# Kernel tuning notes

Measured on AMD Instinct MI355X. Metric: run time of the kernel, lower is better.

Reference implementation:

```python
import jax, jax.numpy as jnp
import numpy as np

B, P, N, H, TD, E = 4, 12, 4096, 64, 128, 65536
EPS = 1e-5


def _layer_norm2d(x, w, b):
    # LayerNorm over last two dims [N, H] with elementwise affine of shape [N, H]
    mu = jnp.mean(x, axis=(-2, -1), keepdims=True)
    var = jnp.var(x, axis=(-2, -1), keepdims=True)
    return (x - mu) * jax.lax.rsqrt(var + EPS) * w + b


def _projection(x, w1, b1, w2, b2):
    return jax.nn.relu(x @ w1.T + b1) @ w2.T + b2


def _lg_conv(x, edge_index):
    # PyG LGConv: symmetric gcn_norm without self loops, then scatter-add.
    row, col = edge_index[0], edge_index[1]
    deg = jax.ops.segment_sum(jnp.ones(E, x.dtype), col, num_segments=N)  # in-degree
    dis = jnp.where(deg > 0, jax.lax.rsqrt(jnp.maximum(deg, 1.0)), 0.0)   # deg^{-1/2}
    norm = dis[row] * dis[col]                                            # [E]
    xt = jnp.moveaxis(x, 2, 0)                                            # [N, B, P, H]
    msgs = xt[row] * norm[:, None, None, None]                            # [E, B, P, H]
    out = jax.ops.segment_sum(msgs, col, num_segments=N)                  # [N, B, P, H]
    return jnp.moveaxis(out, 0, 2)                                        # [B, P, N, H]


def setup_inputs() -> dict:
    key = jax.random.key(0)
    ks = jax.random.split(key, 16)
    s = 0.05
    return {
        "x": jax.random.normal(ks[0], (B, P, N, H), dtype=jnp.float32),
        "edge_index": jax.random.randint(ks[1], (2, E), 0, N),
        "time": jax.random.normal(ks[2], (B, TD), dtype=jnp.float32),
        "cond": jax.random.normal(ks[3], (B, P, N, H), dtype=jnp.float32),
        # time_projection: Linear(TD->H), Linear(H->H)
        "tp_w1": jax.random.normal(ks[4], (H, TD), dtype=jnp.float32) * s,
        "tp_b1": jnp.zeros((H,), jnp.float32),
        "tp_w2": jax.random.normal(ks[5], (H, H), dtype=jnp.float32) * s,
        "tp_b2": jnp.zeros((H,), jnp.float32),
        # cond_projection: Linear(H->H), Linear(H->H)
        "cp_w1": jax.random.normal(ks[6], (H, H), dtype=jnp.float32) * s,
        "cp_b1": jnp.zeros((H,), jnp.float32),
        "cp_w2": jax.random.normal(ks[7], (H, H), dtype=jnp.float32) * s,
        "cp_b2": jnp.zeros((H,), jnp.float32),
        # LayerNorm affine params [N, H]
        "gn_w": jnp.ones((N, H), jnp.float32),
        "gn_b": jnp.zeros((N, H), jnp.float32),
        "tn_w": jnp.ones((N, H), jnp.float32),
        "tn_b": jnp.zeros((N, H), jnp.float32),
        # Conv2d(P, P, 1x1)
        "conv_w": jax.random.normal(ks[8], (P, P), dtype=jnp.float32) * s,
        "conv_b": jnp.zeros((P,), jnp.float32),
    }


def reference(x, edge_index, time, cond, tp_w1, tp_b1, tp_w2, tp_b2,
              cp_w1, cp_b1, cp_w2, cp_b2, gn_w, gn_b, tn_w, tn_b,
              conv_w, conv_b):
    t = _projection(time, tp_w1, tp_b1, tp_w2, tp_b2)[:, None, None, :]  # [B,1,1,H]
    c = _projection(cond, cp_w1, cp_b1, cp_w2, cp_b2)                    # [B,P,N,H]
    h = x + c
    h = _layer_norm2d(h, gn_w, gn_b)
    h = _lg_conv(h, edge_index)
    h = h + t
    h = _layer_norm2d(h, tn_w, tn_b)
    # 1x1 Conv2d over the periods (channel) axis
    h = jnp.einsum('bpnh,qp->bqnh', h, conv_w) + conv_b[None, :, None, None]
    return h
```

## Files before the change

### kernel.cpp

```cpp
#include <hip/hip_runtime.h>
#include <hip/hip_bf16.h>

#define Bc   4
#define Pc   12
#define Nc   4096
#define Hc   64
#define TDc  128
#define Ec   65536
#define BPc  48
#define Gg   6
#define NHc  (Nc*Hc)
#define ROWS (BPc*Nc)
#define EPSc 1e-5f

typedef float    f32x4 __attribute__((ext_vector_type(4)));
typedef _Float16 f16x2 __attribute__((ext_vector_type(2)));
typedef _Float16 f16x4 __attribute__((ext_vector_type(4)));
typedef _Float16 f16x8 __attribute__((ext_vector_type(8)));

__global__ void k_tproj(const float* __restrict__ timev,
                        const float* __restrict__ w1, const float* __restrict__ b1,
                        const float* __restrict__ w2, const float* __restrict__ b2,
                        float* __restrict__ t_out) {
    __shared__ float s_time[Bc * TDc];
    __shared__ float s_hid[Bc * Hc];
    int t = threadIdx.x;
    for (int i = t; i < Bc * TDc; i += 256) s_time[i] = timev[i];
    __syncthreads();
    int b = t >> 6, j = t & 63;
    float acc = b1[j];
    for (int k = 0; k < TDc; ++k) acc = fmaf(s_time[b * TDc + k], w1[j * TDc + k], acc);
    s_hid[b * Hc + j] = fmaxf(acc, 0.f);
    __syncthreads();
    float acc2 = b2[j];
    for (int k = 0; k < Hc; ++k) acc2 = fmaf(s_hid[b * Hc + k], w2[j * Hc + k], acc2);
    t_out[b * Hc + j] = acc2;
}

__global__ void k_deg(const int* __restrict__ col, int* __restrict__ deg) {
    int e = blockIdx.x * 256 + threadIdx.x;
    atomicAdd(&deg[col[e]], 1);
}

__global__ __launch_bounds__(1024) void k_scan(const int* __restrict__ deg,
                                               int* __restrict__ offs,
                                               int* __restrict__ cursor,
                                               float* __restrict__ dis) {
    __shared__ int part[1024];
    int t = threadIdx.x;
    int d0 = deg[t * 4], d1 = deg[t * 4 + 1], d2 = deg[t * 4 + 2], d3 = deg[t * 4 + 3];
    part[t] = d0 + d1 + d2 + d3;
    __syncthreads();
    for (int off = 1; off < 1024; off <<= 1) {
        int v = (t >= off) ? part[t - off] : 0;
        __syncthreads();
        part[t] += v;
        __syncthreads();
    }
    int base = (t ? part[t - 1] : 0);
    offs[t * 4]     = base;
    offs[t * 4 + 1] = base + d0;
    offs[t * 4 + 2] = base + d0 + d1;
    offs[t * 4 + 3] = base + d0 + d1 + d2;
    if (t == 1023) offs[4096] = part[1023];
    cursor[t * 4]     = base;
    cursor[t * 4 + 1] = base + d0;
    cursor[t * 4 + 2] = base + d0 + d1;
    cursor[t * 4 + 3] = base + d0 + d1 + d2;
    dis[t * 4]     = d0 > 0 ? rsqrtf((float)d0) : 0.f;
    dis[t * 4 + 1] = d1 > 0 ? rsqrtf((float)d1) : 0.f;
    dis[t * 4 + 2] = d2 > 0 ? rsqrtf((float)d2) : 0.f;
    dis[t * 4 + 3] = d3 > 0 ? rsqrtf((float)d3) : 0.f;
}

__global__ void k_fill(const int* __restrict__ ei, int* __restrict__ cursor,
                       const float* __restrict__ dis,
                       int2* __restrict__ csr2) {
    int e = blockIdx.x * 256 + threadIdx.x;
    int r = ei[e], c = ei[Ec + e];
    int pos = atomicAdd(&cursor[c], 1);
    int2 v;
    v.x = r;
    v.y = __float_as_int(dis[r] * dis[c]);
    csr2[pos] = v;
}

__global__ __launch_bounds__(256) void k_pack(const float* __restrict__ gnw,
                                              const float* __restrict__ gnb,
                                              f16x2* __restrict__ gpack) {
    int i = blockIdx.x * 256 + threadIdx.x;
    f16x2 v;
    v.x = (_Float16)gnw[i];
    v.y = (_Float16)gnb[i];
    gpack[i] = v;
}

__global__ __launch_bounds__(256) void k_gw(const int* __restrict__ offs,
                                            const int2* __restrict__ csr2,
                                            const f16x2* __restrict__ gpack,
                                            float* __restrict__ g1, float* __restrict__ g2) {
    int wv = threadIdx.x >> 6, lane = threadIdx.x & 63;
    int n = __builtin_amdgcn_readfirstlane(blockIdx.x * 4 + wv);
    int s0 = __builtin_amdgcn_readfirstlane(offs[n]);
    int s1 = __builtin_amdgcn_readfirstlane(offs[n + 1]);
    float a0 = 0.f, a1 = 0.f, a2 = 0.f, a3 = 0.f;
    float b0 = 0.f, b1 = 0.f, b2 = 0.f, b3 = 0.f;
    int i = s0;
    for (; i + 4 <= s1; i += 4) {
        int2 e0 = csr2[i], e1 = csr2[i + 1], e2 = csr2[i + 2], e3 = csr2[i + 3];
        f16x2 v0 = gpack[e0.x * Hc + lane];
        f16x2 v1 = gpack[e1.x * Hc + lane];
        f16x2 v2 = gpack[e2.x * Hc + lane];
        f16x2 v3 = gpack[e3.x * Hc + lane];
        float w0 = __int_as_float(e0.y), w1 = __int_as_float(e1.y);
        float w2 = __int_as_float(e2.y), w3 = __int_as_float(e3.y);
        a0 = fmaf(w0, (float)v0.x, a0); b0 = fmaf(w0, (float)v0.y, b0);
        a1 = fmaf(w1, (float)v1.x, a1); b1 = fmaf(w1, (float)v1.y, b1);
        a2 = fmaf(w2, (float)v2.x, a2); b2 = fmaf(w2, (float)v2.y, b2);
        a3 = fmaf(w3, (float)v3.x, a3); b3 = fmaf(w3, (float)v3.y, b3);
    }
    for (; i < s1; ++i) {
        int2 e = csr2[i];
        f16x2 v = gpack[e.x * Hc + lane];
        float w = __int_as_float(e.y);
        a0 = fmaf(w, (float)v.x, a0); b0 = fmaf(w, (float)v.y, b0);
    }
    g1[n * Hc + lane] = (a0 + a1) + (a2 + a3);
    g2[n * Hc + lane] = (b0 + b1) + (b2 + b3);
}

__global__ __launch_bounds__(256) void k_mlp(const float* __restrict__ cond,
                                             const float* __restrict__ x,
                                             const float* __restrict__ w1, const float* __restrict__ b1,
                                             const float* __restrict__ w2, const float* __restrict__ b2,
                                             const float* __restrict__ gnw,
                                             _Float16* __restrict__ Af, float* __restrict__ part1) {
    __shared__ __align__(16) _Float16 wlds[8192];
    __shared__ float blds[128];
    __shared__ __align__(16) _Float16 s_h[4][16][72];

    int tid  = threadIdx.x;
    int lane = tid & 63;
    int wv   = tid >> 6;
    int r = lane & 15, g = lane >> 4;
    int bp = blockIdx.x >> 5;
    int g4 = bp & 7, j6 = bp >> 3;
    int nbase = (blockIdx.x & 31) * 128;

    #pragma unroll
    for (int layer = 0; layer < 2; ++layer) {
        const float* wsrc = layer ? w2 : w1;
        #pragma unroll
        for (int v4 = 0; v4 < 4; ++v4) {
            int i4 = tid + v4 * 256;
            int j  = i4 >> 4;
            int kq = (i4 & 15) * 4;
            f32x4 v = *(const f32x4*)(wsrc + j * Hc + kq);
            int t = j >> 4, rr = j & 15, kk = kq >> 4, gg = (kq >> 2) & 3;
            int ln = gg * 16 + rr;
            *(f16x4*)&wlds[(((layer * 4 + t) * 4 + kk) * 64 + ln) * 4] =
                __builtin_convertvector(v, f16x4);
        }
    }
    if (tid < 64) blds[tid] = b1[tid];
    else if (tid < 128) blds[tid] = b2[tid - 64];
    __syncthreads();

    float s = 0.f, ss = 0.f;
    int blockRow = blockIdx.x * 128;
    int nl = lane >> 3, hq = (lane & 7) * 8;
    for (int c = 0; c < 2; ++c) {
        __syncthreads();
        int row = blockRow + wv * 32 + c * 16 + r;
        int n   = row & (Nc - 1);
        f32x4 bcf[4], x4[4], gw4[4];
        #pragma unroll
        for (int kk = 0; kk < 4; ++kk)
            bcf[kk] = *(const f32x4*)(cond + (size_t)row * Hc + kk * 16 + 4 * g);
        #pragma unroll
        for (int t = 0; t < 4; ++t) {
            x4[t]  = *(const f32x4*)(x + (size_t)row * Hc + 16 * t + 4 * g);
            gw4[t] = *(const f32x4*)(gnw + n * Hc + 16 * t + 4 * g);
        }
        f16x4 bc[4];
        #pragma unroll
        for (int kk = 0; kk < 4; ++kk) bc[kk] = __builtin_convertvector(bcf[kk], f16x4);
        f16x4 hB[4];
        #pragma unroll
        for (int t = 0; t < 4; ++t) {
            f32x4 acc = {0.f, 0.f, 0.f, 0.f};
            #pragma unroll
            for (int kk = 0; kk < 4; ++kk) {
                f16x4 a = *(const f16x4*)&wlds[((t * 4 + kk) * 64 + lane) * 4];
                acc = __builtin_amdgcn_mfma_f32_16x16x16f16(a, bc[kk], acc, 0, 0, 0);
            }
            acc += *(const f32x4*)&blds[16 * t + 4 * g];
            f32x4 h;
            h.x = fmaxf(acc.x, 0.f); h.y = fmaxf(acc.y, 0.f);
            h.z = fmaxf(acc.z, 0.f); h.w = fmaxf(acc.w, 0.f);
            hB[t] = __builtin_convertvector(h, f16x4);
        }
        #pragma unroll
        for (int t = 0; t < 4; ++t) {
            f32x4 acc = {0.f, 0.f, 0.f, 0.f};
            #pragma unroll
            for (int kk = 0; kk < 4; ++kk) {
                f16x4 a = *(const f16x4*)&wlds[((16 + t * 4 + kk) * 64 + lane) * 4];
                acc = __builtin_amdgcn_mfma_f32_16x16x16f16(a, hB[kk], acc, 0, 0, 0);
            }
            f32x4 o = acc + *(const f32x4*)&blds[64 + 16 * t + 4 * g] + x4[t];
            s  += o.x + o.y + o.z + o.w;
            ss += o.x * o.x + o.y * o.y + o.z * o.z + o.w * o.w;
            f32x4 av = o * gw4[t];
            *(f16x4*)&s_h[wv][r][16 * t + 4 * g] = __builtin_convertvector(av, f16x4);
        }
        #pragma unroll
        for (int p = 0; p < 2; ++p) {
            f16x8 v = *(const f16x8*)&s_h[wv][p * 8 + nl][hq];
            int nn = nbase + wv * 32 + c * 16 + p * 8 + nl;
            *(f16x8*)(Af + (((size_t)g4 * Nc + nn) * Gg + j6) * Hc + hq) = v;
        }
    }
    for (int off = 32; off; off >>= 1) { s += __shfl_down(s, off); ss += __shfl_down(ss, off); }
    if (lane == 0) {
        int idx = (blockIdx.x & 31) * 4 + wv;
        part1[(bp * 128 + idx) * 2]     = s;
        part1[(bp * 128 + idx) * 2 + 1] = ss;
    }
}

__global__ __launch_bounds__(256) void k_finalize(const float* __restrict__ part, int cnt,
                                                  float* __restrict__ murs) {
    int bp = blockIdx.x;
    float s = 0.f, ss = 0.f;
    for (int i = threadIdx.x; i < cnt; i += 256) {
        s  += part[(bp * cnt + i) * 2];
        ss += part[(bp * cnt + i) * 2 + 1];
    }
    __shared__ float ls[4], lss[4];
    for (int off = 32; off; off >>= 1) { s += __shfl_down(s, off); ss += __shfl_down(ss, off); }
    int w = threadIdx.x >> 6, l = threadIdx.x & 63;
    if (l == 0) { ls[w] = s; lss[w] = ss; }
    __syncthreads();
    if (threadIdx.x == 0) {
        s  = ls[0] + ls[1] + ls[2] + ls[3];
        ss = lss[0] + lss[1] + lss[2] + lss[3];
        float mu = s / (float)NHc;
        float var = ss / (float)NHc - mu * mu;
        murs[bp * 2]     = mu;
        murs[bp * 2 + 1] = rsqrtf(var + EPSc);
    }
}

__global__ __launch_bounds__(256) void k_gather(const int* __restrict__ offs,
                                                const int2* __restrict__ csr2,
                                                const _Float16* __restrict__ Af,
                                                const float* __restrict__ g1,
                                                const float* __restrict__ g2,
                                                const float* __restrict__ murs,
                                                const float* __restrict__ t_in,
                                                _Float16* __restrict__ h2f,
                                                float* __restrict__ part2) {
    int bid = blockIdx.x;
    int g   = bid & 7;
    int seq = bid >> 3;
    int wv = threadIdx.x >> 6, lane = threadIdx.x & 63;
    int n  = __builtin_amdgcn_readfirstlane(seq * 4 + wv);
    int jj = lane >> 3;
    int jc = jj < Gg ? jj : 0;
    int h0 = (lane & 7) * 8;
    const _Float16* base = Af + (size_t)g * (Nc * Gg * Hc) + jc * Hc + h0;
    int s0 = __builtin_amdgcn_readfirstlane(offs[n]);
    int s1 = __builtin_amdgcn_readfirstlane(offs[n + 1]);

    float acc[8];
    #pragma unroll
    for (int i = 0; i < 8; ++i) acc[i] = 0.f;

    int idx = s0;
    for (; idx + 4 <= s1; idx += 4) {
        int2 e0 = csr2[idx],     e1 = csr2[idx + 1];
        int2 e2 = csr2[idx + 2], e3 = csr2[idx + 3];
        f16x8 v0 = *(const f16x8*)(base + (size_t)e0.x * (Gg * Hc));
        f16x8 v1 = *(const f16x8*)(base + (size_t)e1.x * (Gg * Hc));
        f16x8 v2 = *(const f16x8*)(base + (size_t)e2.x * (Gg * Hc));
        f16x8 v3 = *(const f16x8*)(base + (size_t)e3.x * (Gg * Hc));
        float w0 = __int_as_float(e0.y), w1 = __int_as_float(e1.y);
        float w2 = __int_as_float(e2.y), w3 = __int_as_float(e3.y);
        #pragma unroll
        for (int i = 0; i < 8; ++i) {
            acc[i] = fmaf(w0, (float)v0[i], acc[i]);
            acc[i] = fmaf(w1, (float)v1[i], acc[i]);
            acc[i] = fmaf(w2, (float)v2[i], acc[i]);
            acc[i] = fmaf(w3, (float)v3[i], acc[i]);
        }
    }
    for (; idx < s1; ++idx) {
        int2 e = csr2[idx];
        f16x8 v = *(const f16x8*)(base + (size_t)e.x * (Gg * Hc));
        float w = __int_as_float(e.y);
        #pragma unroll
        for (int i = 0; i < 8; ++i) acc[i] = fmaf(w, (float)v[i], acc[i]);
    }

    int bp = g + 8 * jc;
    int b  = bp / Pc;
    float mu = murs[bp * 2], rs = murs[bp * 2 + 1];
    f32x4 g1a = *(const f32x4*)(g1 + n * Hc + h0);
    f32x4 g1b = *(const f32x4*)(g1 + n * Hc + h0 + 4);
    f32x4 g2a = *(const f32x4*)(g2 + n * Hc + h0);
    f32x4 g2b = *(const f32x4*)(g2 + n * Hc + h0 + 4);
    f32x4 tta = *(const f32x4*)(t_in + b * Hc + h0);
    f32x4 ttb = *(const f32x4*)(t_in + b * Hc + h0 + 4);
    f32x4 va, vb;
    va.x = rs * (acc[0] - mu * g1a.x) + g2a.x + tta.x;
    va.y = rs * (acc[1] - mu * g1a.y) + g2a.y + tta.y;
    va.z = rs * (acc[2] - mu * g1a.z) + g2a.z + tta.z;
    va.w = rs * (acc[3] - mu * g1a.w) + g2a.w + tta.w;
    vb.x = rs * (acc[4] - mu * g1b.x) + g2b.x + ttb.x;
    vb.y = rs * (acc[5] - mu * g1b.y) + g2b.y + ttb.y;
    vb.z = rs * (acc[6] - mu * g1b.z) + g2b.z + ttb.z;
    vb.w = rs * (acc[7] - mu * g1b.w) + g2b.w + ttb.w;

    float s  = (va.x + va.y) + (va.z + va.w) + (vb.x + vb.y) + (vb.z + vb.w);
    float ss = va.x * va.x + va.y * va.y + va.z * va.z + va.w * va.w
             + vb.x * vb.x + vb.y * vb.y + vb.z * vb.z + vb.w * vb.w;
    #pragma unroll
    for (int m = 4; m; m >>= 1) { s += __shfl_xor(s, m); ss += __shfl_xor(ss, m); }

    if (jj < Gg) {
        f16x8 hv;
        hv[0] = (_Float16)va.x; hv[1] = (_Float16)va.y;
        hv[2] = (_Float16)va.z; hv[3] = (_Float16)va.w;
        hv[4] = (_Float16)vb.x; hv[5] = (_Float16)vb.y;
        hv[6] = (_Float16)vb.z; hv[7] = (_Float16)vb.w;
        *(f16x8*)(h2f + (size_t)bp * NHc + n * Hc + h0) = hv;
        if ((lane & 7) == 0) {
            part2[((size_t)bp * Nc + n) * 2]     = s;
            part2[((size_t)bp * Nc + n) * 2 + 1] = ss;
        }
    }
}

__global__ __launch_bounds__(256) void k_conv(const _Float16* __restrict__ h2f,
                                              const float* __restrict__ murs,
                                              const float* __restrict__ tnw, const float* __restrict__ tnb,
                                              const float* __restrict__ cw, const float* __restrict__ cb,
                                              float* __restrict__ out) {
    int tid = blockIdx.x * 256 + threadIdx.x;
    int b  = tid >> 16;
    int i4 = tid & 65535;
    size_t e0 = (size_t)i4 * 4;
    float4 w4 = *(const float4*)(tnw + e0);
    float4 b4 = *(const float4*)(tnb + e0);
    float v[Pc][4];
    #pragma unroll
    for (int p = 0; p < Pc; ++p) {
        int bp = b * Pc + p;
        float mu = murs[bp * 2], rs = murs[bp * 2 + 1];
        f16x4 h = *(const f16x4*)(h2f + (size_t)bp * NHc + e0);
        v[p][0] = ((float)h.x - mu) * rs * w4.x + b4.x;
        v[p][1] = ((float)h.y - mu) * rs * w4.y + b4.y;
        v[p][2] = ((float)h.z - mu) * rs * w4.z + b4.z;
        v[p][3] = ((float)h.w - mu) * rs * w4.w + b4.w;
    }
    #pragma unroll
    for (int q = 0; q < Pc; ++q) {
        float cbq = cb[q];
        float o0 = cbq, o1 = cbq, o2 = cbq, o3 = cbq;
        #pragma unroll
        for (int p = 0; p < Pc; ++p) {
            float wqp = cw[q * Pc + p];
            o0 = fmaf(v[p][0], wqp, o0);
            o1 = fmaf(v[p][1], wqp, o1);
            o2 = fmaf(v[p][2], wqp, o2);
            o3 = fmaf(v[p][3], wqp, o3);
        }
        float4 o = {o0, o1, o2, o3};
        *(float4*)(out + (size_t)(b * Pc + q) * NHc + e0) = o;
    }
}

extern "C" void kernel_launch(void* const* d_in, const int* in_sizes, int n_in,
                              void* d_out, int out_size, void* d_ws, size_t ws_size,
                              hipStream_t stream) {
    (void)in_sizes; (void)n_in; (void)out_size; (void)ws_size;
    const float* x     = (const float*)d_in[0];
    const int*   ei    = (const int*)  d_in[1];
    const float* timev = (const float*)d_in[2];
    const float* cond  = (const float*)d_in[3];
    const float* tp_w1 = (const float*)d_in[4];
    const float* tp_b1 = (const float*)d_in[5];
    const float* tp_w2 = (const float*)d_in[6];
    const float* tp_b2 = (const float*)d_in[7];
    const float* cp_w1 = (const float*)d_in[8];
    const float* cp_b1 = (const float*)d_in[9];
    const float* cp_w2 = (const float*)d_in[10];
    const float* cp_b2 = (const float*)d_in[11];
    const float* gn_w  = (const float*)d_in[12];
    const float* gn_b  = (const float*)d_in[13];
    const float* tn_w  = (const float*)d_in[14];
    const float* tn_b  = (const float*)d_in[15];
    const float* cw    = (const float*)d_in[16];
    const float* cb    = (const float*)d_in[17];
    float* out = (float*)d_out;

    char* w = (char*)d_ws;
    size_t off = 0;
    auto alloc = [&](size_t bytes) {
        void* p = w + off;
        off = (off + bytes + 255) & ~(size_t)255;
        return p;
    };
    _Float16* Af   = (_Float16*)alloc((size_t)ROWS * Hc * sizeof(_Float16));
    _Float16* h2f  = (_Float16*)alloc((size_t)ROWS * Hc * sizeof(_Float16));
    float* part1   = (float*)alloc((size_t)BPc * 128 * 2 * 4);
    float* part2   = (float*)alloc((size_t)BPc * Nc * 2 * 4);
    float* murs1   = (float*)alloc(96 * 4);
    float* murs2   = (float*)alloc(96 * 4);
    float* t_ws    = (float*)alloc(256 * 4);
    float* dis     = (float*)alloc(Nc * 4);
    int2*  csr2    = (int2*)alloc((size_t)Ec * 8);
    float* g1      = (float*)alloc((size_t)NHc * 4);
    float* g2      = (float*)alloc((size_t)NHc * 4);
    f16x2* gpack   = (f16x2*)alloc((size_t)NHc * 4);
    int*   deg     = (int*)alloc(Nc * 4);
    int*   offs    = (int*)alloc((Nc + 1) * 4);
    int*   cursor  = (int*)alloc(Nc * 4);

    hipMemsetAsync(deg, 0, Nc * sizeof(int), stream);
    k_tproj<<<1, 256, 0, stream>>>(timev, tp_w1, tp_b1, tp_w2, tp_b2, t_ws);
    k_deg<<<Ec / 256, 256, 0, stream>>>(ei + Ec, deg);
    k_scan<<<1, 1024, 0, stream>>>(deg, offs, cursor, dis);
    k_fill<<<Ec / 256, 256, 0, stream>>>(ei, cursor, dis, csr2);
    k_pack<<<NHc / 256, 256, 0, stream>>>(gn_w, gn_b, gpack);
    k_gw<<<Nc / 4, 256, 0, stream>>>(offs, csr2, gpack, g1, g2);
    k_mlp<<<ROWS / 128, 256, 0, stream>>>(cond, x, cp_w1, cp_b1, cp_w2, cp_b2, gn_w, Af, part1);
    k_finalize<<<BPc, 256, 0, stream>>>(part1, 128, murs1);
    k_gather<<<8 * 1024, 256, 0, stream>>>(offs, csr2, Af, g1, g2,
                                           murs1, t_ws, h2f, part2);
    k_finalize<<<BPc, 256, 0, stream>>>(part2, Nc, murs2);
    k_conv<<<(Bc * NHc / 4) / 256, 256, 0, stream>>>(h2f, murs2, tn_w, tn_b, cw, cb, out);
}
```

Before: 116.8 us.

## Merge prep kernels and fold first stats finalize into MLP via last-block reduction

Merges the time projection, the gn weight/bias packing and the degree zeroing (formerly a memset) into one multi-role prep kernel. The first LayerNorm statistics finalize moves into the tail of the MLP kernel using an atomic counter and a last-block-done reduction. The gather kernel now skips the neighbor loop for the idle lanes (jj >= 6) instead of computing on a clamped index. Together these cut about three launches from the stream, at the cost of an atomic, extra fences and a serial finalize in one block.

```diff
diff --git a/kernel.cpp b/kernel.cpp
--- a/kernel.cpp
+++ b/kernel.cpp
@@ -18,23 +18,41 @@
 typedef _Float16 f16x4 __attribute__((ext_vector_type(4)));
 typedef _Float16 f16x8 __attribute__((ext_vector_type(8)));
 
-__global__ void k_tproj(const float* __restrict__ timev,
-                        const float* __restrict__ w1, const float* __restrict__ b1,
-                        const float* __restrict__ w2, const float* __restrict__ b2,
-                        float* __restrict__ t_out) {
-    __shared__ float s_time[Bc * TDc];
-    __shared__ float s_hid[Bc * Hc];
+__global__ __launch_bounds__(256) void k_prep(const float* __restrict__ timev,
+                                              const float* __restrict__ w1, const float* __restrict__ b1,
+                                              const float* __restrict__ w2, const float* __restrict__ b2,
+                                              float* __restrict__ t_out,
+                                              const float* __restrict__ gnw,
+                                              const float* __restrict__ gnb,
+                                              f16x2* __restrict__ gpack,
+                                              int* __restrict__ deg,
+                                              int* __restrict__ counter) {
+    int bid = blockIdx.x;
     int t = threadIdx.x;
-    for (int i = t; i < Bc * TDc; i += 256) s_time[i] = timev[i];
-    __syncthreads();
-    int b = t >> 6, j = t & 63;
-    float acc = b1[j];
-    for (int k = 0; k < TDc; ++k) acc = fmaf(s_time[b * TDc + k], w1[j * TDc + k], acc);
-    s_hid[b * Hc + j] = fmaxf(acc, 0.f);
-    __syncthreads();
-    float acc2 = b2[j];
-    for (int k = 0; k < Hc; ++k) acc2 = fmaf(s_hid[b * Hc + k], w2[j * Hc + k], acc2);
-    t_out[b * Hc + j] = acc2;
+    if (bid == 0) {
+        __shared__ float s_time[Bc * TDc];
+        __shared__ float s_hid[Bc * Hc];
+        for (int i = t; i < Bc * TDc; i += 256) s_time[i] = timev[i];
+        __syncthreads();
+        int b = t >> 6, j = t & 63;
+        float acc = b1[j];
+        for (int k = 0; k < TDc; ++k) acc = fmaf(s_time[b * TDc + k], w1[j * TDc + k], acc);
+        s_hid[b * Hc + j] = fmaxf(acc, 0.f);
+        __syncthreads();
+        float acc2 = b2[j];
+        for (int k = 0; k < Hc; ++k) acc2 = fmaf(s_hid[b * Hc + k], w2[j * Hc + k], acc2);
+        t_out[b * Hc + j] = acc2;
+    } else if (bid <= 1024) {
+        int i = (bid - 1) * 256 + t;
+        f16x2 v;
+        v.x = (_Float16)gnw[i];
+        v.y = (_Float16)gnb[i];
+        gpack[i] = v;
+    } else {
+        int i = (bid - 1025) * 256 + t;
+        if (i < Nc) deg[i] = 0;
+        if (bid == 1025 && t == 0) counter[0] = 0;
+    }
 }
 
 __global__ void k_deg(const int* __restrict__ col, int* __restrict__ deg) {
@@ -83,16 +101,6 @@
     v.x = r;
     v.y = __float_as_int(dis[r] * dis[c]);
     csr2[pos] = v;
-}
-
-__global__ __launch_bounds__(256) void k_pack(const float* __restrict__ gnw,
-                                              const float* __restrict__ gnb,
-                                              f16x2* __restrict__ gpack) {
-    int i = blockIdx.x * 256 + threadIdx.x;
-    f16x2 v;
-    v.x = (_Float16)gnw[i];
-    v.y = (_Float16)gnb[i];
-    gpack[i] = v;
 }
 
 __global__ __launch_bounds__(256) void k_gw(const int* __restrict__ offs,
@@ -134,10 +142,12 @@
                                              const float* __restrict__ w1, const float* __restrict__ b1,
                                              const float* __restrict__ w2, const float* __restrict__ b2,
                                              const float* __restrict__ gnw,
-                                             _Float16* __restrict__ Af, float* __restrict__ part1) {
+                                             _Float16* __restrict__ Af, float* __restrict__ part1,
+                                             float* __restrict__ murs1, int* __restrict__ counter) {
     __shared__ __align__(16) _Float16 wlds[8192];
     __shared__ float blds[128];
     __shared__ __align__(16) _Float16 s_h[4][16][72];
+    __shared__ int s_last;
 
     int tid  = threadIdx.x;
     int lane = tid & 63;
@@ -226,6 +236,33 @@
         int idx = (blockIdx.x & 31) * 4 + wv;
         part1[(bp * 128 + idx) * 2]     = s;
         part1[(bp * 128 + idx) * 2 + 1] = ss;
+    }
+
+    __syncthreads();
+    if (tid == 0) {
+        __threadfence();
+        int done = atomicAdd(counter, 1);
+        s_last = (done == (int)gridDim.x - 1);
+    }
+    __syncthreads();
+    if (s_last) {
+        __threadfence();
+        if (tid < 192) {
+            int bpp = tid >> 2, j = tid & 3;
+            float fs = 0.f, fss = 0.f;
+            for (int i = j; i < 128; i += 4) {
+                fs  += part1[(bpp * 128 + i) * 2];
+                fss += part1[(bpp * 128 + i) * 2 + 1];
+            }
+            fs += __shfl_down(fs, 2); fss += __shfl_down(fss, 2);
+            fs += __shfl_down(fs, 1); fss += __shfl_down(fss, 1);
+            if (j == 0) {
+                float mu = fs / (float)NHc;
+                float var = fss / (float)NHc - mu * mu;
+                murs1[bpp * 2]     = mu;
+                murs1[bpp * 2 + 1] = rsqrtf(var + EPSc);
+            }
+        }
     }
 }
 
@@ -267,68 +304,67 @@
     int wv = threadIdx.x >> 6, lane = threadIdx.x & 63;
     int n  = __builtin_amdgcn_readfirstlane(seq * 4 + wv);
     int jj = lane >> 3;
-    int jc = jj < Gg ? jj : 0;
     int h0 = (lane & 7) * 8;
-    const _Float16* base = Af + (size_t)g * (Nc * Gg * Hc) + jc * Hc + h0;
     int s0 = __builtin_amdgcn_readfirstlane(offs[n]);
     int s1 = __builtin_amdgcn_readfirstlane(offs[n + 1]);
 
-    float acc[8];
-    #pragma unroll
-    for (int i = 0; i < 8; ++i) acc[i] = 0.f;
-
-    int idx = s0;
-    for (; idx + 4 <= s1; idx += 4) {
-        int2 e0 = csr2[idx],     e1 = csr2[idx + 1];
-        int2 e2 = csr2[idx + 2], e3 = csr2[idx + 3];
-        f16x8 v0 = *(const f16x8*)(base + (size_t)e0.x * (Gg * Hc));
-        f16x8 v1 = *(const f16x8*)(base + (size_t)e1.x * (Gg * Hc));
-        f16x8 v2 = *(const f16x8*)(base + (size_t)e2.x * (Gg * Hc));
-        f16x8 v3 = *(const f16x8*)(base + (size_t)e3.x * (Gg * Hc));
-        float w0 = __int_as_float(e0.y), w1 = __int_as_float(e1.y);
-        float w2 = __int_as_float(e2.y), w3 = __int_as_float(e3.y);
-        #pragma unroll
-        for (int i = 0; i < 8; ++i) {
-            acc[i] = fmaf(w0, (float)v0[i], acc[i]);
-            acc[i] = fmaf(w1, (float)v1[i], acc[i]);
-            acc[i] = fmaf(w2, (float)v2[i], acc[i]);
-            acc[i] = fmaf(w3, (float)v3[i], acc[i]);
-        }
-    }
-    for (; idx < s1; ++idx) {
-        int2 e = csr2[idx];
-        f16x8 v = *(const f16x8*)(base + (size_t)e.x * (Gg * Hc));
-        float w = __int_as_float(e.y);
-        #pragma unroll
-        for (int i = 0; i < 8; ++i) acc[i] = fmaf(w, (float)v[i], acc[i]);
-    }
-
-    int bp = g + 8 * jc;
-    int b  = bp / Pc;
-    float mu = murs[bp * 2], rs = murs[bp * 2 + 1];
-    f32x4 g1a = *(const f32x4*)(g1 + n * Hc + h0);
-    f32x4 g1b = *(const f32x4*)(g1 + n * Hc + h0 + 4);
-    f32x4 g2a = *(const f32x4*)(g2 + n * Hc + h0);
-    f32x4 g2b = *(const f32x4*)(g2 + n * Hc + h0 + 4);
-    f32x4 tta = *(const f32x4*)(t_in + b * Hc + h0);
-    f32x4 ttb = *(const f32x4*)(t_in + b * Hc + h0 + 4);
-    f32x4 va, vb;
-    va.x = rs * (acc[0] - mu * g1a.x) + g2a.x + tta.x;
-    va.y = rs * (acc[1] - mu * g1a.y) + g2a.y + tta.y;
-    va.z = rs * (acc[2] - mu * g1a.z) + g2a.z + tta.z;
-    va.w = rs * (acc[3] - mu * g1a.w) + g2a.w + tta.w;
-    vb.x = rs * (acc[4] - mu * g1b.x) + g2b.x + ttb.x;
-    vb.y = rs * (acc[5] - mu * g1b.y) + g2b.y + ttb.y;
-    vb.z = rs * (acc[6] - mu * g1b.z) + g2b.z + ttb.z;
-    vb.w = rs * (acc[7] - mu * g1b.w) + g2b.w + ttb.w;
-
-    float s  = (va.x + va.y) + (va.z + va.w) + (vb.x + vb.y) + (vb.z + vb.w);
-    float ss = va.x * va.x + va.y * va.y + va.z * va.z + va.w * va.w
-             + vb.x * vb.x + vb.y * vb.y + vb.z * vb.z + vb.w * vb.w;
-    #pragma unroll
-    for (int m = 4; m; m >>= 1) { s += __shfl_xor(s, m); ss += __shfl_xor(ss, m); }
-
     if (jj < Gg) {
+        const _Float16* base = Af + (size_t)g * (Nc * Gg * Hc) + jj * Hc + h0;
+        float acc[8];
+        #pragma unroll
+        for (int i = 0; i < 8; ++i) acc[i] = 0.f;
+
+        int idx = s0;
+        for (; idx + 4 <= s1; idx += 4) {
+            int2 e0 = csr2[idx],     e1 = csr2[idx + 1];
+            int2 e2 = csr2[idx + 2], e3 = csr2[idx + 3];
+            f16x8 v0 = *(const f16x8*)(base + (size_t)e0.x * (Gg * Hc));
+            f16x8 v1 = *(const f16x8*)(base + (size_t)e1.x * (Gg * Hc));
+            f16x8 v2 = *(const f16x8*)(base + (size_t)e2.x * (Gg * Hc));
+            f16x8 v3 = *(const f16x8*)(base + (size_t)e3.x * (Gg * Hc));
+            float w0 = __int_as_float(e0.y), w1 = __int_as_float(e1.y);
+            float w2 = __int_as_float(e2.y), w3 = __int_as_float(e3.y);
+            #pragma unroll
+            for (int i = 0; i < 8; ++i) {
+                acc[i] = fmaf(w0, (float)v0[i], acc[i]);
+                acc[i] = fmaf(w1, (float)v1[i], acc[i]);
+                acc[i] = fmaf(w2, (float)v2[i], acc[i]);
+                acc[i] = fmaf(w3, (float)v3[i], acc[i]);
+            }
+        }
+        for (; idx < s1; ++idx) {
+            int2 e = csr2[idx];
+            f16x8 v = *(const f16x8*)(base + (size_t)e.x * (Gg * Hc));
+            float w = __int_as_float(e.y);
+            #pragma unroll
+            for (int i = 0; i < 8; ++i) acc[i] = fmaf(w, (float)v[i], acc[i]);
+        }
+
+        int bp = g + 8 * jj;
+        int b  = bp / Pc;
+        float mu = murs[bp * 2], rs = murs[bp * 2 + 1];
+        f32x4 g1a = *(const f32x4*)(g1 + n * Hc + h0);
+        f32x4 g1b = *(const f32x4*)(g1 + n * Hc + h0 + 4);
+        f32x4 g2a = *(const f32x4*)(g2 + n * Hc + h0);
+        f32x4 g2b = *(const f32x4*)(g2 + n * Hc + h0 + 4);
+        f32x4 tta = *(const f32x4*)(t_in + b * Hc + h0);
+        f32x4 ttb = *(const f32x4*)(t_in + b * Hc + h0 + 4);
+        f32x4 va, vb;
+        va.x = rs * (acc[0] - mu * g1a.x) + g2a.x + tta.x;
+        va.y = rs * (acc[1] - mu * g1a.y) + g2a.y + tta.y;
+        va.z = rs * (acc[2] - mu * g1a.z) + g2a.z + tta.z;
+        va.w = rs * (acc[3] - mu * g1a.w) + g2a.w + tta.w;
+        vb.x = rs * (acc[4] - mu * g1b.x) + g2b.x + ttb.x;
+        vb.y = rs * (acc[5] - mu * g1b.y) + g2b.y + ttb.y;
+        vb.z = rs * (acc[6] - mu * g1b.z) + g2b.z + ttb.z;
+        vb.w = rs * (acc[7] - mu * g1b.w) + g2b.w + ttb.w;
+
+        float s  = (va.x + va.y) + (va.z + va.w) + (vb.x + vb.y) + (vb.z + vb.w);
+        float ss = va.x * va.x + va.y * va.y + va.z * va.z + va.w * va.w
+                 + vb.x * vb.x + vb.y * vb.y + vb.z * vb.z + vb.w * vb.w;
+        #pragma unroll
+        for (int m = 4; m; m >>= 1) { s += __shfl_xor(s, m); ss += __shfl_xor(ss, m); }
+
         f16x8 hv;
         hv[0] = (_Float16)va.x; hv[1] = (_Float16)va.y;
         hv[2] = (_Float16)va.z; hv[3] = (_Float16)va.w;
@@ -427,16 +463,16 @@
     int*   deg     = (int*)alloc(Nc * 4);
     int*   offs    = (int*)alloc((Nc + 1) * 4);
     int*   cursor  = (int*)alloc(Nc * 4);
-
-    hipMemsetAsync(deg, 0, Nc * sizeof(int), stream);
-    k_tproj<<<1, 256, 0, stream>>>(timev, tp_w1, tp_b1, tp_w2, tp_b2, t_ws);
+    int*   counter = (int*)alloc(256);
+
+    k_prep<<<1041, 256, 0, stream>>>(timev, tp_w1, tp_b1, tp_w2, tp_b2, t_ws,
+                                     gn_w, gn_b, gpack, deg, counter);
     k_deg<<<Ec / 256, 256, 0, stream>>>(ei + Ec, deg);
     k_scan<<<1, 1024, 0, stream>>>(deg, offs, cursor, dis);
     k_fill<<<Ec / 256, 256, 0, stream>>>(ei, cursor, dis, csr2);
-    k_pack<<<NHc / 256, 256, 0, stream>>>(gn_w, gn_b, gpack);
     k_gw<<<Nc / 4, 256, 0, stream>>>(offs, csr2, gpack, g1, g2);
-    k_mlp<<<ROWS / 128, 256, 0, stream>>>(cond, x, cp_w1, cp_b1, cp_w2, cp_b2, gn_w, Af, part1);
-    k_finalize<<<BPc, 256, 0, stream>>>(part1, 128, murs1);
+    k_mlp<<<ROWS / 128, 256, 0, stream>>>(cond, x, cp_w1, cp_b1, cp_w2, cp_b2, gn_w,
+                                          Af, part1, murs1, counter);
     k_gather<<<8 * 1024, 256, 0, stream>>>(offs, csr2, Af, g1, g2,
                                            murs1, t_ws, h2f, part2);
     k_finalize<<<BPc, 256, 0, stream>>>(part2, Nc, murs2);
```

New measurement: 165.2 us. 41.5% more time.
